# Kernel optimization log

Measured on AMD Instinct MI355X. Metric: run time of the kernel, lower is better.

Reference implementation:

```python
import jax, jax.numpy as jnp
import numpy as np

HIDDEN = 1024
HEADS = 16
HEAD_DIM = HIDDEN // HEADS
ROPE_BASE = 10000.0


def setup_inputs() -> dict:
    key = jax.random.key(0)
    ks = jax.random.split(key, 5)
    B, S = 2, 2048
    x = jax.random.normal(ks[0], (B, S, HIDDEN), dtype=jnp.float32)
    Wqkv_w = jax.random.normal(ks[1], (3 * HIDDEN, HIDDEN), dtype=jnp.float32) * 0.02
    Wqkv_b = jax.random.normal(ks[2], (3 * HIDDEN,), dtype=jnp.float32) * 0.02
    out_w = jax.random.normal(ks[3], (HIDDEN, HIDDEN), dtype=jnp.float32) * 0.02
    out_b = jax.random.normal(ks[4], (HIDDEN,), dtype=jnp.float32) * 0.02
    return {"x": x, "Wqkv_w": Wqkv_w, "Wqkv_b": Wqkv_b, "out_w": out_w, "out_b": out_b}


def _rope_cos_sin(seqlen, dtype):
    inv_freq = 1.0 / (ROPE_BASE ** (jnp.arange(0, HEAD_DIM, 2, dtype=jnp.float32) / HEAD_DIM))
    t = jnp.arange(seqlen, dtype=jnp.float32)
    freqs = jnp.outer(t, inv_freq)                      # [S, D/2]
    emb = jnp.concatenate([freqs, freqs], axis=-1)      # [S, D]
    return jnp.cos(emb).astype(dtype), jnp.sin(emb).astype(dtype)


def _rotate_half(x):
    half = x.shape[-1] // 2
    return jnp.concatenate([-x[..., half:], x[..., :half]], axis=-1)


def reference(x, Wqkv_w, Wqkv_b, out_w, out_b):
    B, S, _ = x.shape
    qkv = x @ Wqkv_w.T + Wqkv_b                          # [B,S,3*H*D]
    qkv = qkv.reshape(B, S, 3, HEADS, HEAD_DIM)
    q, k, v = qkv[:, :, 0], qkv[:, :, 1], qkv[:, :, 2]   # [B,S,H,D]
    cos, sin = _rope_cos_sin(S, x.dtype)
    cos = cos[None, :, None, :]                          # [1,S,1,D]
    sin = sin[None, :, None, :]
    q = q * cos + _rotate_half(q) * sin
    k = k * cos + _rotate_half(k) * sin
    # SDPA (no mask, non-causal): softmax(q k^T / sqrt(D)) v
    scale = 1.0 / jnp.sqrt(jnp.asarray(HEAD_DIM, dtype=x.dtype))
    scores = jnp.einsum('bqhd,bkhd->bhqk', q, k) * scale # [B,H,S,S]
    probs = jax.nn.softmax(scores, axis=-1)
    out = jnp.einsum('bhqk,bkhd->bqhd', probs, v)        # [B,S,H,D]
    out = out.reshape(B, S, HEADS * HEAD_DIM)
    return out @ out_w.T + out_b
```

## Files before the change

kernel.cpp:

```cpp
#include <hip/hip_runtime.h>
#include <hip/hip_bf16.h>
#include <cstdint>

#define HIDDEN 1024
#define HEADS 16
#define HDIM 64
#define BATCH 2
#define SEQ 2048

typedef __attribute__((ext_vector_type(8))) short bfrag;
typedef __attribute__((ext_vector_type(4))) float f32x4;

__device__ inline unsigned short f2bf(float f) {
  unsigned u = __float_as_uint(f);
  return (unsigned short)((u + 0x7FFFu + ((u >> 16) & 1u)) >> 16);
}

__device__ inline void split2(float f, unsigned short& h, unsigned short& l) {
  unsigned u = __float_as_uint(f);
  unsigned hb = (u + 0x7FFFu + ((u >> 16) & 1u)) & 0xFFFF0000u;
  h = (unsigned short)(hb >> 16);
  l = f2bf(f - __uint_as_float(hb));
}

__device__ inline void split8(float4 a, float4 b, float scale, bfrag& hi, bfrag& lo) {
  float v[8] = {a.x, a.y, a.z, a.w, b.x, b.y, b.z, b.w};
  bfrag h, l;
#pragma unroll
  for (int e = 0; e < 8; e++) {
    unsigned short hh, ll;
    split2(v[e] * scale, hh, ll);
    h[e] = (short)hh; l[e] = (short)ll;
  }
  hi = h; lo = l;
}

__global__ __launch_bounds__(256) void rope_table_k(float* __restrict__ ctab,
                                                    float* __restrict__ stab) {
  int idx = blockIdx.x * 256 + threadIdx.x;
  int s = idx >> 5, i = idx & 31;
  float inv = powf(10000.0f, -(float)i / 32.0f);
  float a = (float)s * inv;
  ctab[idx] = cosf(a);
  stab[idx] = sinf(a);
}

__global__ __launch_bounds__(256, 2) void gemm_mfma3(
    const float* __restrict__ A, const float* __restrict__ B,
    const float* __restrict__ bias, float* __restrict__ Cout,
    float* __restrict__ Qb, float* __restrict__ Kb, float* __restrict__ Vb,
    int N, int K, int mode) {
  __shared__ __align__(16) unsigned short Ah[128 * 64];
  __shared__ __align__(16) unsigned short Al[128 * 64];
  __shared__ __align__(16) unsigned short Bh[128 * 64];
  __shared__ __align__(16) unsigned short Bl[128 * 64];

  const int t = threadIdx.x;
  const int lane = t & 63, wv = t >> 6;
  const int wm = wv >> 1, wn = wv & 1;
  const int fr = lane & 15, fg = lane >> 4;
  const int n0 = blockIdx.x * 128, m0 = blockIdx.y * 128;

  f32x4 acc[4][4];
#pragma unroll
  for (int i = 0; i < 4; i++)
#pragma unroll
    for (int j = 0; j < 4; j++) acc[i][j] = (f32x4){0.f, 0.f, 0.f, 0.f};

  float4 fA[4][2], fB[4][2];
#pragma unroll
  for (int it = 0; it < 4; it++) {
    int flat = it * 256 + t, r = flat >> 3, g = flat & 7;
    const float* pa = A + (size_t)(m0 + r) * K + g * 8;
    const float* pb = B + (size_t)(n0 + r) * K + g * 8;
    fA[it][0] = *(const float4*)pa; fA[it][1] = *(const float4*)(pa + 4);
    fB[it][0] = *(const float4*)pb; fB[it][1] = *(const float4*)(pb + 4);
  }

  for (int kt = 0; kt < K; kt += 64) {
    __syncthreads();
#pragma unroll
    for (int it = 0; it < 4; it++) {
      int flat = it * 256 + t, r = flat >> 3, g = flat & 7;
      int ad = r * 64 + ((g ^ (r & 7)) << 3);
      bfrag ha, la, hb, lb;
      split8(fA[it][0], fA[it][1], 1.0f, ha, la);
      split8(fB[it][0], fB[it][1], 1.0f, hb, lb);
      *(bfrag*)&Ah[ad] = ha;
      *(bfrag*)&Al[ad] = la;
      *(bfrag*)&Bh[ad] = hb;
      *(bfrag*)&Bl[ad] = lb;
    }
    __syncthreads();

    if (kt + 64 < K) {
#pragma unroll
      for (int it = 0; it < 4; it++) {
        int flat = it * 256 + t, r = flat >> 3, g = flat & 7;
        const float* pa = A + (size_t)(m0 + r) * K + kt + 64 + g * 8;
        const float* pb = B + (size_t)(n0 + r) * K + kt + 64 + g * 8;
        fA[it][0] = *(const float4*)pa; fA[it][1] = *(const float4*)(pa + 4);
        fB[it][0] = *(const float4*)pb; fB[it][1] = *(const float4*)(pb + 4);
      }
    }

#pragma unroll
    for (int kk = 0; kk < 2; kk++) {
      bfrag ah[4], al[4], bh[4], bl[4];
#pragma unroll
      for (int i = 0; i < 4; i++) {
        int r = wm * 64 + i * 16 + fr;
        int ad = r * 64 + (((kk * 4 + fg) ^ (r & 7)) << 3);
        ah[i] = *(const bfrag*)&Ah[ad];
        al[i] = *(const bfrag*)&Al[ad];
      }
#pragma unroll
      for (int j = 0; j < 4; j++) {
        int r = wn * 64 + j * 16 + fr;
        int ad = r * 64 + (((kk * 4 + fg) ^ (r & 7)) << 3);
        bh[j] = *(const bfrag*)&Bh[ad];
        bl[j] = *(const bfrag*)&Bl[ad];
      }
#pragma unroll
      for (int i = 0; i < 4; i++)
#pragma unroll
        for (int j = 0; j < 4; j++) {
          acc[i][j] = __builtin_amdgcn_mfma_f32_16x16x32_bf16(ah[i], bh[j], acc[i][j], 0, 0, 0);
          acc[i][j] = __builtin_amdgcn_mfma_f32_16x16x32_bf16(ah[i], bl[j], acc[i][j], 0, 0, 0);
          acc[i][j] = __builtin_amdgcn_mfma_f32_16x16x32_bf16(al[i], bh[j], acc[i][j], 0, 0, 0);
        }
    }
  }

#pragma unroll
  for (int j = 0; j < 4; j++) {
    const int n = n0 + wn * 64 + j * 16 + fr;
    const float bb = bias[n];
#pragma unroll
    for (int i = 0; i < 4; i++) {
#pragma unroll
      for (int reg = 0; reg < 4; reg++) {
        const int m = m0 + wm * 64 + i * 16 + fg * 4 + reg;
        const float val = acc[i][j][reg] + bb;
        if (mode == 0) {
          Cout[(size_t)m * N + n] = val;
        } else {
          const int which = n >> 10;
          const int h = (n >> 6) & (HEADS - 1);
          const int d = n & (HDIM - 1);
          const int b = m >> 11, s = m & (SEQ - 1);
          float* base = (which == 0) ? Qb : ((which == 1) ? Kb : Vb);
          base[(((size_t)(b * HEADS + h)) * SEQ + s) * HDIM + d] = val;
        }
      }
    }
  }
}

__global__ __launch_bounds__(256) void rope_apply_k(float* __restrict__ Qb,
                                                    float* __restrict__ Kb,
                                                    const float* __restrict__ ctab,
                                                    const float* __restrict__ stab) {
  int idx = blockIdx.x * 256 + threadIdx.x;
  float* P = blockIdx.y ? Kb : Qb;
  int c4 = (idx & 7) * 4;
  int row = idx >> 3;
  int s = row & (SEQ - 1);
  float* p0 = P + (size_t)row * HDIM + c4;
  float4 lo = *(float4*)p0;
  float4 hi = *(float4*)(p0 + 32);
  float4 cc = *(const float4*)(ctab + s * 32 + c4);
  float4 ss = *(const float4*)(stab + s * 32 + c4);
  float4 nlo, nhi;
  nlo.x = lo.x * cc.x - hi.x * ss.x;  nhi.x = hi.x * cc.x + lo.x * ss.x;
  nlo.y = lo.y * cc.y - hi.y * ss.y;  nhi.y = hi.y * cc.y + lo.y * ss.y;
  nlo.z = lo.z * cc.z - hi.z * ss.z;  nhi.z = hi.z * cc.z + lo.z * ss.z;
  nlo.w = lo.w * cc.w - hi.w * ss.w;  nhi.w = hi.w * cc.w + lo.w * ss.w;
  *(float4*)p0 = nlo;
  *(float4*)(p0 + 32) = nhi;
}

__global__ __launch_bounds__(256, 2) void attn_mfma(
    const float* __restrict__ Qb, const float* __restrict__ Kb,
    const float* __restrict__ Vb, float* __restrict__ Ob) {
  __shared__ __align__(16) unsigned short Kh[64 * 64], Kl[64 * 64];
  __shared__ __align__(16) unsigned short Vth[64 * 64], Vtl[64 * 64];
  __shared__ __align__(16) unsigned short Ph[128 * 64], Pl[128 * 64];

  const int t = threadIdx.x;
  const int lane = t & 63, w = t >> 6;
  const int fr = lane & 15, fg = lane >> 4;
  const int q0 = blockIdx.x * 128;
  const int h = blockIdx.y, b = blockIdx.z;
  const size_t hb = ((size_t)(b * HEADS + h)) * SEQ * HDIM;
  const float* Qp = Qb + hb;
  const float* Kp = Kb + hb;
  const float* Vp = Vb + hb;

  bfrag qh[2][2], ql[2][2];
#pragma unroll
  for (int qf = 0; qf < 2; qf++)
#pragma unroll
    for (int kk = 0; kk < 2; kk++) {
      const float* p = Qp + (size_t)(q0 + w * 32 + qf * 16 + fr) * HDIM + kk * 32 + fg * 8;
      split8(*(const float4*)p, *(const float4*)(p + 4), 0.125f, qh[qf][kk], ql[qf][kk]);
    }

  f32x4 Oacc[2][4];
#pragma unroll
  for (int qf = 0; qf < 2; qf++)
#pragma unroll
    for (int df = 0; df < 4; df++) Oacc[qf][df] = (f32x4){0.f, 0.f, 0.f, 0.f};
  float m_i[2] = {-1e30f, -1e30f}, l_i[2] = {0.f, 0.f};

  for (int kt = 0; kt < SEQ; kt += 64) {
    __syncthreads();
#pragma unroll
    for (int c = 0; c < 2; c++) {
      int flat = c * 256 + t, row = flat >> 3, g = flat & 7;
      const float* p = Kp + (size_t)(kt + row) * HDIM + g * 8;
      bfrag hh, ll;
      split8(*(const float4*)p, *(const float4*)(p + 4), 1.0f, hh, ll);
      int ad = row * 64 + ((g ^ (row & 7)) << 3);
      *(bfrag*)&Kh[ad] = hh;
      *(bfrag*)&Kl[ad] = ll;
    }
#pragma unroll
    for (int c = 0; c < 2; c++) {
      int flat = c * 256 + t, key = flat >> 3, dq = flat & 7;
      const float* p = Vp + (size_t)(kt + key) * HDIM + dq * 8;
      float4 x0 = *(const float4*)p, x1 = *(const float4*)(p + 4);
      float v[8] = {x0.x, x0.y, x0.z, x0.w, x1.x, x1.y, x1.z, x1.w};
#pragma unroll
      for (int e = 0; e < 8; e++) {
        int d = dq * 8 + e;
        unsigned short hh, ll;
        split2(v[e], hh, ll);
        int gs = ((key >> 3) ^ (d & 7) ^ ((d >> 3) & 7)) & 7;
        int ad = d * 64 + gs * 8 + (key & 7);
        Vth[ad] = hh;
        Vtl[ad] = ll;
      }
    }
    __syncthreads();

    f32x4 sacc[4][2];
#pragma unroll
    for (int ki = 0; ki < 4; ki++)
#pragma unroll
      for (int qf = 0; qf < 2; qf++) sacc[ki][qf] = (f32x4){0.f, 0.f, 0.f, 0.f};
#pragma unroll
    for (int kk = 0; kk < 2; kk++) {
      bfrag kh[4], kl[4];
#pragma unroll
      for (int ki = 0; ki < 4; ki++) {
        int row = ki * 16 + fr;
        int ad = row * 64 + (((4 * kk + fg) ^ (row & 7)) << 3);
        kh[ki] = *(const bfrag*)&Kh[ad];
        kl[ki] = *(const bfrag*)&Kl[ad];
      }
#pragma unroll
      for (int ki = 0; ki < 4; ki++)
#pragma unroll
        for (int qf = 0; qf < 2; qf++) {
          sacc[ki][qf] = __builtin_amdgcn_mfma_f32_16x16x32_bf16(kh[ki], qh[qf][kk], sacc[ki][qf], 0, 0, 0);
          sacc[ki][qf] = __builtin_amdgcn_mfma_f32_16x16x32_bf16(kh[ki], ql[qf][kk], sacc[ki][qf], 0, 0, 0);
          sacc[ki][qf] = __builtin_amdgcn_mfma_f32_16x16x32_bf16(kl[ki], qh[qf][kk], sacc[ki][qf], 0, 0, 0);
        }
    }

#pragma unroll
    for (int qf = 0; qf < 2; qf++) {
      float mm = -1e30f;
#pragma unroll
      for (int ki = 0; ki < 4; ki++)
#pragma unroll
        for (int r = 0; r < 4; r++) mm = fmaxf(mm, sacc[ki][qf][r]);
      mm = fmaxf(mm, __shfl_xor(mm, 16));
      mm = fmaxf(mm, __shfl_xor(mm, 32));
      float mn = fmaxf(m_i[qf], mm);
      float alpha = __expf(m_i[qf] - mn);
      m_i[qf] = mn;
      float rs = 0.f;
      float pv[4][4];
#pragma unroll
      for (int ki = 0; ki < 4; ki++)
#pragma unroll
        for (int r = 0; r < 4; r++) {
          float p = __expf(sacc[ki][qf][r] - mn);
          pv[ki][r] = p;
          rs += p;
        }
      rs += __shfl_xor(rs, 16);
      rs += __shfl_xor(rs, 32);
      l_i[qf] = l_i[qf] * alpha + rs;

      int qrow = w * 32 + qf * 16 + fr;
#pragma unroll
      for (int ki = 0; ki < 4; ki++) {
        unsigned short hh[4], ll[4];
#pragma unroll
        for (int r = 0; r < 4; r++) split2(pv[ki][r], hh[r], ll[r]);
        int key0 = ki * 16 + 4 * fg;
        int ads = qrow * 64 + (((key0 >> 3) ^ (qrow & 7)) << 3) + (key0 & 7);
        *(uint2*)&Ph[ads] = make_uint2((unsigned)hh[0] | ((unsigned)hh[1] << 16),
                                       (unsigned)hh[2] | ((unsigned)hh[3] << 16));
        *(uint2*)&Pl[ads] = make_uint2((unsigned)ll[0] | ((unsigned)ll[1] << 16),
                                       (unsigned)ll[2] | ((unsigned)ll[3] << 16));
      }
      float ar[4];
#pragma unroll
      for (int r = 0; r < 4; r++) ar[r] = __shfl(alpha, 4 * fg + r);
#pragma unroll
      for (int df = 0; df < 4; df++)
#pragma unroll
        for (int r = 0; r < 4; r++) Oacc[qf][df][r] *= ar[r];
    }

#pragma unroll
    for (int kk = 0; kk < 2; kk++) {
      bfrag pa[2], pb[2], vh[4], vl[4];
#pragma unroll
      for (int qf = 0; qf < 2; qf++) {
        int qrow = w * 32 + qf * 16 + fr;
        int ad = qrow * 64 + (((4 * kk + fg) ^ (qrow & 7)) << 3);
        pa[qf] = *(const bfrag*)&Ph[ad];
        pb[qf] = *(const bfrag*)&Pl[ad];
      }
#pragma unroll
      for (int df = 0; df < 4; df++) {
        int d = df * 16 + fr;
        int gs = ((4 * kk + fg) ^ (d & 7) ^ ((d >> 3) & 7)) & 7;
        int ad = d * 64 + gs * 8;
        vh[df] = *(const bfrag*)&Vth[ad];
        vl[df] = *(const bfrag*)&Vtl[ad];
      }
#pragma unroll
      for (int qf = 0; qf < 2; qf++)
#pragma unroll
        for (int df = 0; df < 4; df++) {
          Oacc[qf][df] = __builtin_amdgcn_mfma_f32_16x16x32_bf16(pa[qf], vh[df], Oacc[qf][df], 0, 0, 0);
          Oacc[qf][df] = __builtin_amdgcn_mfma_f32_16x16x32_bf16(pa[qf], vl[df], Oacc[qf][df], 0, 0, 0);
          Oacc[qf][df] = __builtin_amdgcn_mfma_f32_16x16x32_bf16(pb[qf], vh[df], Oacc[qf][df], 0, 0, 0);
        }
    }
  }

#pragma unroll
  for (int qf = 0; qf < 2; qf++) {
    float lr[4];
#pragma unroll
    for (int r = 0; r < 4; r++) lr[r] = 1.0f / __shfl(l_i[qf], 4 * fg + r);
#pragma unroll
    for (int df = 0; df < 4; df++)
#pragma unroll
      for (int r = 0; r < 4; r++) {
        int s = q0 + w * 32 + qf * 16 + 4 * fg + r;
        int d = df * 16 + fr;
        Ob[(((size_t)(b * SEQ + s)) * HEADS + h) * HDIM + d] = Oacc[qf][df][r] * lr[r];
      }
  }
}

extern "C" void kernel_launch(void* const* d_in, const int* in_sizes, int n_in,
                              void* d_out, int out_size, void* d_ws, size_t ws_size,
                              hipStream_t stream) {
  const float* x    = (const float*)d_in[0];
  const float* Wqkv = (const float*)d_in[1];
  const float* bqkv = (const float*)d_in[2];
  const float* Wout = (const float*)d_in[3];
  const float* bout = (const float*)d_in[4];
  float* out = (float*)d_out;

  float* ws = (float*)d_ws;
  const size_t HSZ = (size_t)BATCH * HEADS * SEQ * HDIM;
  float* ctab = ws;
  float* stab = ctab + SEQ * 32;
  float* Qb = stab + SEQ * 32;
  float* Kb = Qb + HSZ;
  float* Vb = Kb + HSZ;
  float* Ab = Vb + HSZ;

  hipLaunchKernelGGL(rope_table_k, dim3(SEQ * 32 / 256), dim3(256), 0, stream,
                     ctab, stab);
  hipLaunchKernelGGL(gemm_mfma3, dim3(3 * HIDDEN / 128, BATCH * SEQ / 128),
                     dim3(256), 0, stream,
                     x, Wqkv, bqkv, (float*)nullptr, Qb, Kb, Vb,
                     3 * HIDDEN, HIDDEN, 1);
  hipLaunchKernelGGL(rope_apply_k, dim3(BATCH * HEADS * SEQ * 8 / 256, 2),
                     dim3(256), 0, stream, Qb, Kb, ctab, stab);
  hipLaunchKernelGGL(attn_mfma, dim3(SEQ / 128, HEADS, BATCH), dim3(256), 0, stream,
                     Qb, Kb, Vb, Ab);
  hipLaunchKernelGGL(gemm_mfma3, dim3(HIDDEN / 128, BATCH * SEQ / 128),
                     dim3(256), 0, stream,
                     Ab, Wout, bout, out, (float*)nullptr, (float*)nullptr,
                     (float*)nullptr, HIDDEN, HIDDEN, 0);
}
```

Baseline: 386.6 us.

## Pre-split operands to bf16 hi/lo buffers and stream tiles via global_load_lds

Adds standalone passes that split fp32 inputs, weights, rope-rotated Q/K and a transposed V into swizzled bf16 hi/lo arrays. The GEMM and attention kernels can then load tiles straight into LDS with global_load_lds instead of converting in the main loop. Attention now keeps P in registers, packed with v_cvt_pk_bf16, and feeds it to 16x16x16 MFMAs or lane shuffles instead of staging it in LDS. The GEMM K-tile shrinks to 32 and occupancy rises to 3 blocks per CU. The cost is extra launches and extra global memory traffic for the split buffers, and the weights are re-split on every call.

```diff
diff --git a/kernel.cpp b/kernel.cpp
--- a/kernel.cpp
+++ b/kernel.cpp
@@ -9,30 +9,39 @@
 #define SEQ 2048
 
 typedef __attribute__((ext_vector_type(8))) short bfrag;
+typedef __attribute__((ext_vector_type(4))) short bhalf4;
 typedef __attribute__((ext_vector_type(4))) float f32x4;
+
+union U4B { uint4 u; bfrag b; };
+union U2B { uint2 u; bhalf4 b; };
+
+#if defined(__has_builtin)
+#if __has_builtin(__builtin_amdgcn_mfma_f32_16x16x16bf16_1k)
+#define MFMA16(a, b, c) __builtin_amdgcn_mfma_f32_16x16x16bf16_1k(a, b, c, 0, 0, 0)
+#elif __has_builtin(__builtin_amdgcn_mfma_f32_16x16x16_bf16)
+#define MFMA16(a, b, c) __builtin_amdgcn_mfma_f32_16x16x16_bf16(a, b, c, 0, 0, 0)
+#endif
+#endif
 
 __device__ inline unsigned short f2bf(float f) {
   unsigned u = __float_as_uint(f);
   return (unsigned short)((u + 0x7FFFu + ((u >> 16) & 1u)) >> 16);
 }
-
 __device__ inline void split2(float f, unsigned short& h, unsigned short& l) {
   unsigned u = __float_as_uint(f);
   unsigned hb = (u + 0x7FFFu + ((u >> 16) & 1u)) & 0xFFFF0000u;
   h = (unsigned short)(hb >> 16);
   l = f2bf(f - __uint_as_float(hb));
 }
-
-__device__ inline void split8(float4 a, float4 b, float scale, bfrag& hi, bfrag& lo) {
-  float v[8] = {a.x, a.y, a.z, a.w, b.x, b.y, b.z, b.w};
-  bfrag h, l;
-#pragma unroll
-  for (int e = 0; e < 8; e++) {
-    unsigned short hh, ll;
-    split2(v[e] * scale, hh, ll);
-    h[e] = (short)hh; l[e] = (short)ll;
-  }
-  hi = h; lo = l;
+__device__ inline unsigned cvt_pk_bf16(float a, float b) {
+  unsigned d;
+  asm("v_cvt_pk_bf16_f32 %0, %1, %2" : "=v"(d) : "v"(a), "v"(b));
+  return d;
+}
+__device__ inline void gll16(const void* g, void* l) {
+  __builtin_amdgcn_global_load_lds(
+      (const __attribute__((address_space(1))) void*)g,
+      (__attribute__((address_space(3))) void*)l, 16, 0, 0);
 }
 
 __global__ __launch_bounds__(256) void rope_table_k(float* __restrict__ ctab,
@@ -45,20 +54,39 @@
   stab[idx] = sinf(a);
 }
 
-__global__ __launch_bounds__(256, 2) void gemm_mfma3(
-    const float* __restrict__ A, const float* __restrict__ B,
+__global__ __launch_bounds__(256) void split_swz4(const float* __restrict__ in,
+                                                  ushort* __restrict__ ph,
+                                                  ushort* __restrict__ pl) {
+  int gid = blockIdx.x * 256 + threadIdx.x;
+  int r = gid >> 7, g = gid & 127;
+  const float* p = in + (size_t)r * 1024 + g * 8;
+  float4 a = *(const float4*)p, b = *(const float4*)(p + 4);
+  float v[8] = {a.x, a.y, a.z, a.w, b.x, b.y, b.z, b.w};
+  unsigned hw[4], lw[4];
+#pragma unroll
+  for (int i = 0; i < 4; i++) {
+    unsigned short h0, l0, h1, l1;
+    split2(v[2 * i], h0, l0);
+    split2(v[2 * i + 1], h1, l1);
+    hw[i] = (unsigned)h0 | ((unsigned)h1 << 16);
+    lw[i] = (unsigned)l0 | ((unsigned)l1 << 16);
+  }
+  size_t dst = (size_t)r * 1024 + (g >> 2) * 32 +
+               ((((g & 3) ^ (r & 3) ^ ((r >> 2) & 3))) << 3);
+  *(uint4*)(ph + dst) = make_uint4(hw[0], hw[1], hw[2], hw[3]);
+  *(uint4*)(pl + dst) = make_uint4(lw[0], lw[1], lw[2], lw[3]);
+}
+
+__global__ __launch_bounds__(256, 3) void gemm32(
+    const ushort* __restrict__ aph, const ushort* __restrict__ apl,
+    const ushort* __restrict__ bph, const ushort* __restrict__ bpl,
     const float* __restrict__ bias, float* __restrict__ Cout,
     float* __restrict__ Qb, float* __restrict__ Kb, float* __restrict__ Vb,
-    int N, int K, int mode) {
-  __shared__ __align__(16) unsigned short Ah[128 * 64];
-  __shared__ __align__(16) unsigned short Al[128 * 64];
-  __shared__ __align__(16) unsigned short Bh[128 * 64];
-  __shared__ __align__(16) unsigned short Bl[128 * 64];
-
-  const int t = threadIdx.x;
-  const int lane = t & 63, wv = t >> 6;
-  const int wm = wv >> 1, wn = wv & 1;
-  const int fr = lane & 15, fg = lane >> 4;
+    int N, int mode) {
+  __shared__ __align__(16) ushort Ah[128 * 32], Al[128 * 32];
+  __shared__ __align__(16) ushort Bh[128 * 32], Bl[128 * 32];
+  const int t = threadIdx.x, lane = t & 63, w = t >> 6;
+  const int wm = w >> 1, wn = w & 1, fr = lane & 15, fg = lane >> 4;
   const int n0 = blockIdx.x * 128, m0 = blockIdx.y * 128;
 
   f32x4 acc[4][4];
@@ -67,68 +95,40 @@
 #pragma unroll
     for (int j = 0; j < 4; j++) acc[i][j] = (f32x4){0.f, 0.f, 0.f, 0.f};
 
-  float4 fA[4][2], fB[4][2];
-#pragma unroll
-  for (int it = 0; it < 4; it++) {
-    int flat = it * 256 + t, r = flat >> 3, g = flat & 7;
-    const float* pa = A + (size_t)(m0 + r) * K + g * 8;
-    const float* pb = B + (size_t)(n0 + r) * K + g * 8;
-    fA[it][0] = *(const float4*)pa; fA[it][1] = *(const float4*)(pa + 4);
-    fB[it][0] = *(const float4*)pb; fB[it][1] = *(const float4*)(pb + 4);
-  }
-
-  for (int kt = 0; kt < K; kt += 64) {
+  const ushort* pl4 = (w == 0) ? aph : (w == 1) ? apl : (w == 2) ? bph : bpl;
+  ushort* ld4 = (w == 0) ? Ah : (w == 1) ? Al : (w == 2) ? Bh : Bl;
+  const int rb = (w < 2) ? m0 : n0;
+
+  for (int kt = 0; kt < 1024; kt += 32) {
     __syncthreads();
 #pragma unroll
-    for (int it = 0; it < 4; it++) {
-      int flat = it * 256 + t, r = flat >> 3, g = flat & 7;
-      int ad = r * 64 + ((g ^ (r & 7)) << 3);
-      bfrag ha, la, hb, lb;
-      split8(fA[it][0], fA[it][1], 1.0f, ha, la);
-      split8(fB[it][0], fB[it][1], 1.0f, hb, lb);
-      *(bfrag*)&Ah[ad] = ha;
-      *(bfrag*)&Al[ad] = la;
-      *(bfrag*)&Bh[ad] = hb;
-      *(bfrag*)&Bl[ad] = lb;
+    for (int i = 0; i < 8; i++) {
+      const ushort* src = pl4 + (size_t)(rb + i * 16 + (lane >> 2)) * 1024 +
+                          kt + ((lane & 3) << 3);
+      gll16(src, &ld4[i * 512]);
     }
     __syncthreads();
 
-    if (kt + 64 < K) {
-#pragma unroll
-      for (int it = 0; it < 4; it++) {
-        int flat = it * 256 + t, r = flat >> 3, g = flat & 7;
-        const float* pa = A + (size_t)(m0 + r) * K + kt + 64 + g * 8;
-        const float* pb = B + (size_t)(n0 + r) * K + kt + 64 + g * 8;
-        fA[it][0] = *(const float4*)pa; fA[it][1] = *(const float4*)(pa + 4);
-        fB[it][0] = *(const float4*)pb; fB[it][1] = *(const float4*)(pb + 4);
-      }
-    }
-
-#pragma unroll
-    for (int kk = 0; kk < 2; kk++) {
-      bfrag ah[4], al[4], bh[4], bl[4];
+    bfrag ah[4], al[4];
+#pragma unroll
+    for (int i = 0; i < 4; i++) {
+      int r = wm * 64 + i * 16 + fr;
+      int ad = r * 32 + ((fg ^ (r & 3) ^ ((r >> 2) & 3)) << 3);
+      ah[i] = *(const bfrag*)&Ah[ad];
+      al[i] = *(const bfrag*)&Al[ad];
+    }
+#pragma unroll
+    for (int j = 0; j < 4; j++) {
+      int r = wn * 64 + j * 16 + fr;
+      int ad = r * 32 + ((fg ^ (r & 3) ^ ((r >> 2) & 3)) << 3);
+      bfrag bh = *(const bfrag*)&Bh[ad];
+      bfrag bl = *(const bfrag*)&Bl[ad];
 #pragma unroll
       for (int i = 0; i < 4; i++) {
-        int r = wm * 64 + i * 16 + fr;
-        int ad = r * 64 + (((kk * 4 + fg) ^ (r & 7)) << 3);
-        ah[i] = *(const bfrag*)&Ah[ad];
-        al[i] = *(const bfrag*)&Al[ad];
-      }
-#pragma unroll
-      for (int j = 0; j < 4; j++) {
-        int r = wn * 64 + j * 16 + fr;
-        int ad = r * 64 + (((kk * 4 + fg) ^ (r & 7)) << 3);
-        bh[j] = *(const bfrag*)&Bh[ad];
-        bl[j] = *(const bfrag*)&Bl[ad];
-      }
-#pragma unroll
-      for (int i = 0; i < 4; i++)
-#pragma unroll
-        for (int j = 0; j < 4; j++) {
-          acc[i][j] = __builtin_amdgcn_mfma_f32_16x16x32_bf16(ah[i], bh[j], acc[i][j], 0, 0, 0);
-          acc[i][j] = __builtin_amdgcn_mfma_f32_16x16x32_bf16(ah[i], bl[j], acc[i][j], 0, 0, 0);
-          acc[i][j] = __builtin_amdgcn_mfma_f32_16x16x32_bf16(al[i], bh[j], acc[i][j], 0, 0, 0);
-        }
+        acc[i][j] = __builtin_amdgcn_mfma_f32_16x16x32_bf16(ah[i], bh, acc[i][j], 0, 0, 0);
+        acc[i][j] = __builtin_amdgcn_mfma_f32_16x16x32_bf16(ah[i], bl, acc[i][j], 0, 0, 0);
+        acc[i][j] = __builtin_amdgcn_mfma_f32_16x16x32_bf16(al[i], bh, acc[i][j], 0, 0, 0);
+      }
     }
   }
 
@@ -157,53 +157,121 @@
   }
 }
 
-__global__ __launch_bounds__(256) void rope_apply_k(float* __restrict__ Qb,
-                                                    float* __restrict__ Kb,
-                                                    const float* __restrict__ ctab,
-                                                    const float* __restrict__ stab) {
+__global__ __launch_bounds__(256) void rope_split_k(
+    const float* __restrict__ Qb, const float* __restrict__ Kb,
+    const float* __restrict__ ctab, const float* __restrict__ stab,
+    ushort* __restrict__ Qh, ushort* __restrict__ Ql,
+    ushort* __restrict__ Kh, ushort* __restrict__ Kl) {
   int idx = blockIdx.x * 256 + threadIdx.x;
-  float* P = blockIdx.y ? Kb : Qb;
-  int c4 = (idx & 7) * 4;
-  int row = idx >> 3;
+  int row = idx >> 2, dq = idx & 3;
+  int d0 = dq * 8;
   int s = row & (SEQ - 1);
-  float* p0 = P + (size_t)row * HDIM + c4;
-  float4 lo = *(float4*)p0;
-  float4 hi = *(float4*)(p0 + 32);
-  float4 cc = *(const float4*)(ctab + s * 32 + c4);
-  float4 ss = *(const float4*)(stab + s * 32 + c4);
-  float4 nlo, nhi;
-  nlo.x = lo.x * cc.x - hi.x * ss.x;  nhi.x = hi.x * cc.x + lo.x * ss.x;
-  nlo.y = lo.y * cc.y - hi.y * ss.y;  nhi.y = hi.y * cc.y + lo.y * ss.y;
-  nlo.z = lo.z * cc.z - hi.z * ss.z;  nhi.z = hi.z * cc.z + lo.z * ss.z;
-  nlo.w = lo.w * cc.w - hi.w * ss.w;  nhi.w = hi.w * cc.w + lo.w * ss.w;
-  *(float4*)p0 = nlo;
-  *(float4*)(p0 + 32) = nhi;
-}
-
-__global__ __launch_bounds__(256, 2) void attn_mfma(
-    const float* __restrict__ Qb, const float* __restrict__ Kb,
-    const float* __restrict__ Vb, float* __restrict__ Ob) {
-  __shared__ __align__(16) unsigned short Kh[64 * 64], Kl[64 * 64];
-  __shared__ __align__(16) unsigned short Vth[64 * 64], Vtl[64 * 64];
-  __shared__ __align__(16) unsigned short Ph[128 * 64], Pl[128 * 64];
-
+  const bool isQ = (blockIdx.y == 0);
+  const float* P = (isQ ? Qb : Kb) + (size_t)row * 64;
+  float4 a0 = *(const float4*)(P + d0), a1 = *(const float4*)(P + d0 + 4);
+  float4 b0 = *(const float4*)(P + d0 + 32), b1 = *(const float4*)(P + d0 + 36);
+  float4 c0 = *(const float4*)(ctab + s * 32 + d0), c1 = *(const float4*)(ctab + s * 32 + d0 + 4);
+  float4 s0 = *(const float4*)(stab + s * 32 + d0), s1 = *(const float4*)(stab + s * 32 + d0 + 4);
+  float lo[8] = {a0.x, a0.y, a0.z, a0.w, a1.x, a1.y, a1.z, a1.w};
+  float hi[8] = {b0.x, b0.y, b0.z, b0.w, b1.x, b1.y, b1.z, b1.w};
+  float cc[8] = {c0.x, c0.y, c0.z, c0.w, c1.x, c1.y, c1.z, c1.w};
+  float ss[8] = {s0.x, s0.y, s0.z, s0.w, s1.x, s1.y, s1.z, s1.w};
+  const float sc = isQ ? 0.125f : 1.0f;
+  unsigned lh[4], ll[4], hh[4], hl[4];
+#pragma unroll
+  for (int i = 0; i < 4; i++) {
+    float n0a = (lo[2 * i] * cc[2 * i] - hi[2 * i] * ss[2 * i]) * sc;
+    float n0b = (lo[2 * i + 1] * cc[2 * i + 1] - hi[2 * i + 1] * ss[2 * i + 1]) * sc;
+    float n1a = (hi[2 * i] * cc[2 * i] + lo[2 * i] * ss[2 * i]) * sc;
+    float n1b = (hi[2 * i + 1] * cc[2 * i + 1] + lo[2 * i + 1] * ss[2 * i + 1]) * sc;
+    unsigned short x0, y0, x1, y1;
+    split2(n0a, x0, y0); split2(n0b, x1, y1);
+    lh[i] = (unsigned)x0 | ((unsigned)x1 << 16);
+    ll[i] = (unsigned)y0 | ((unsigned)y1 << 16);
+    split2(n1a, x0, y0); split2(n1b, x1, y1);
+    hh[i] = (unsigned)x0 | ((unsigned)x1 << 16);
+    hl[i] = (unsigned)y0 | ((unsigned)y1 << 16);
+  }
+  size_t base = (size_t)row * 64;
+  if (isQ) {
+    *(uint4*)(Qh + base + d0) = make_uint4(lh[0], lh[1], lh[2], lh[3]);
+    *(uint4*)(Ql + base + d0) = make_uint4(ll[0], ll[1], ll[2], ll[3]);
+    *(uint4*)(Qh + base + d0 + 32) = make_uint4(hh[0], hh[1], hh[2], hh[3]);
+    *(uint4*)(Ql + base + d0 + 32) = make_uint4(hl[0], hl[1], hl[2], hl[3]);
+  } else {
+    int glo = (dq ^ (s & 7)) << 3;
+    int ghi = ((dq + 4) ^ (s & 7)) << 3;
+    *(uint4*)(Kh + base + glo) = make_uint4(lh[0], lh[1], lh[2], lh[3]);
+    *(uint4*)(Kl + base + glo) = make_uint4(ll[0], ll[1], ll[2], ll[3]);
+    *(uint4*)(Kh + base + ghi) = make_uint4(hh[0], hh[1], hh[2], hh[3]);
+    *(uint4*)(Kl + base + ghi) = make_uint4(hl[0], hl[1], hl[2], hl[3]);
+  }
+}
+
+__global__ __launch_bounds__(256) void vtrans_split(const float* __restrict__ Vb,
+                                                    ushort* __restrict__ Vth,
+                                                    ushort* __restrict__ Vtl) {
+  __shared__ float ftile[64][65];
   const int t = threadIdx.x;
-  const int lane = t & 63, w = t >> 6;
+  const int kt = blockIdx.x, bh = blockIdx.y;
+  {
+    int s_loc = t >> 2, dc = (t & 3) * 16;
+    const float* p = Vb + ((size_t)(bh * SEQ) + kt * 64 + s_loc) * 64 + dc;
+#pragma unroll
+    for (int j = 0; j < 4; j++) {
+      float4 v = *(const float4*)(p + j * 4);
+      ftile[s_loc][dc + j * 4 + 0] = v.x;
+      ftile[s_loc][dc + j * 4 + 1] = v.y;
+      ftile[s_loc][dc + j * 4 + 2] = v.z;
+      ftile[s_loc][dc + j * 4 + 3] = v.w;
+    }
+  }
+  __syncthreads();
+  int d = t >> 2, sc = (t & 3) * 16;
+  size_t rowb = ((size_t)(bh * 64 + d)) * SEQ + kt * 64;
+#pragma unroll
+  for (int jg = 0; jg < 2; jg++) {
+    unsigned hw[4], lw[4];
+#pragma unroll
+    for (int i = 0; i < 4; i++) {
+      unsigned short h0, l0, h1, l1;
+      split2(ftile[sc + jg * 8 + 2 * i][d], h0, l0);
+      split2(ftile[sc + jg * 8 + 2 * i + 1][d], h1, l1);
+      hw[i] = (unsigned)h0 | ((unsigned)h1 << 16);
+      lw[i] = (unsigned)l0 | ((unsigned)l1 << 16);
+    }
+    int gsrc = ((sc >> 3) + jg) & 7;
+    int swz = (gsrc ^ (d & 7) ^ ((d >> 3) & 7)) << 3;
+    *(uint4*)(Vth + rowb + swz) = make_uint4(hw[0], hw[1], hw[2], hw[3]);
+    *(uint4*)(Vtl + rowb + swz) = make_uint4(lw[0], lw[1], lw[2], lw[3]);
+  }
+}
+
+__global__ __launch_bounds__(256, 3) void attn_mfma2(
+    const ushort* __restrict__ Qh, const ushort* __restrict__ Ql,
+    const ushort* __restrict__ Kh, const ushort* __restrict__ Kl,
+    const ushort* __restrict__ Vth, const ushort* __restrict__ Vtl,
+    float* __restrict__ Ab) {
+  __shared__ __align__(16) ushort Ks_h[64 * 64], Ks_l[64 * 64];
+  __shared__ __align__(16) ushort Vs_h[64 * 64], Vs_l[64 * 64];
+
+  const int t = threadIdx.x, lane = t & 63, w = t >> 6;
   const int fr = lane & 15, fg = lane >> 4;
   const int q0 = blockIdx.x * 128;
   const int h = blockIdx.y, b = blockIdx.z;
-  const size_t hb = ((size_t)(b * HEADS + h)) * SEQ * HDIM;
-  const float* Qp = Qb + hb;
-  const float* Kp = Kb + hb;
-  const float* Vp = Vb + hb;
+  const int bh = b * HEADS + h;
 
   bfrag qh[2][2], ql[2][2];
 #pragma unroll
   for (int qf = 0; qf < 2; qf++)
 #pragma unroll
     for (int kk = 0; kk < 2; kk++) {
-      const float* p = Qp + (size_t)(q0 + w * 32 + qf * 16 + fr) * HDIM + kk * 32 + fg * 8;
-      split8(*(const float4*)p, *(const float4*)(p + 4), 0.125f, qh[qf][kk], ql[qf][kk]);
+      size_t off = ((size_t)bh * SEQ + q0 + w * 32 + qf * 16 + fr) * 64 + kk * 32 + fg * 8;
+      U4B uh, ul;
+      uh.u = *(const uint4*)(Qh + off);
+      ul.u = *(const uint4*)(Ql + off);
+      qh[qf][kk] = uh.b;
+      ql[qf][kk] = ul.b;
     }
 
   f32x4 Oacc[2][4];
@@ -213,33 +281,26 @@
     for (int df = 0; df < 4; df++) Oacc[qf][df] = (f32x4){0.f, 0.f, 0.f, 0.f};
   float m_i[2] = {-1e30f, -1e30f}, l_i[2] = {0.f, 0.f};
 
+  const int srcA = fr + ((fg & 1) << 5);
+  const int kisel = fg >> 1;
+
   for (int kt = 0; kt < SEQ; kt += 64) {
     __syncthreads();
-#pragma unroll
-    for (int c = 0; c < 2; c++) {
-      int flat = c * 256 + t, row = flat >> 3, g = flat & 7;
-      const float* p = Kp + (size_t)(kt + row) * HDIM + g * 8;
-      bfrag hh, ll;
-      split8(*(const float4*)p, *(const float4*)(p + 4), 1.0f, hh, ll);
-      int ad = row * 64 + ((g ^ (row & 7)) << 3);
-      *(bfrag*)&Kh[ad] = hh;
-      *(bfrag*)&Kl[ad] = ll;
-    }
-#pragma unroll
-    for (int c = 0; c < 2; c++) {
-      int flat = c * 256 + t, key = flat >> 3, dq = flat & 7;
-      const float* p = Vp + (size_t)(kt + key) * HDIM + dq * 8;
-      float4 x0 = *(const float4*)p, x1 = *(const float4*)(p + 4);
-      float v[8] = {x0.x, x0.y, x0.z, x0.w, x1.x, x1.y, x1.z, x1.w};
-#pragma unroll
-      for (int e = 0; e < 8; e++) {
-        int d = dq * 8 + e;
-        unsigned short hh, ll;
-        split2(v[e], hh, ll);
-        int gs = ((key >> 3) ^ (d & 7) ^ ((d >> 3) & 7)) & 7;
-        int ad = d * 64 + gs * 8 + (key & 7);
-        Vth[ad] = hh;
-        Vtl[ad] = ll;
+    if (w < 2) {
+      const ushort* p = w ? Kl : Kh;
+      ushort* ld = w ? Ks_l : Ks_h;
+#pragma unroll
+      for (int i = 0; i < 8; i++) {
+        const ushort* src = p + ((size_t)bh * SEQ + kt + i * 8 + (lane >> 3)) * 64 + ((lane & 7) << 3);
+        gll16(src, &ld[i * 512]);
+      }
+    } else {
+      const ushort* p = (w == 3) ? Vtl : Vth;
+      ushort* ld = (w == 3) ? Vs_l : Vs_h;
+#pragma unroll
+      for (int i = 0; i < 8; i++) {
+        const ushort* src = p + ((size_t)(bh * 64) + i * 8 + (lane >> 3)) * SEQ + kt + ((lane & 7) << 3);
+        gll16(src, &ld[i * 512]);
       }
     }
     __syncthreads();
@@ -251,24 +312,26 @@
       for (int qf = 0; qf < 2; qf++) sacc[ki][qf] = (f32x4){0.f, 0.f, 0.f, 0.f};
 #pragma unroll
     for (int kk = 0; kk < 2; kk++) {
-      bfrag kh[4], kl[4];
 #pragma unroll
       for (int ki = 0; ki < 4; ki++) {
-        int row = ki * 16 + fr;
-        int ad = row * 64 + (((4 * kk + fg) ^ (row & 7)) << 3);
-        kh[ki] = *(const bfrag*)&Kh[ad];
-        kl[ki] = *(const bfrag*)&Kl[ad];
-      }
-#pragma unroll
-      for (int ki = 0; ki < 4; ki++)
+        int r = ki * 16 + fr;
+        int ad = r * 64 + (((kk * 4 + fg) ^ (r & 7)) << 3);
+        bfrag kh = *(const bfrag*)&Ks_h[ad];
+        bfrag kl = *(const bfrag*)&Ks_l[ad];
 #pragma unroll
         for (int qf = 0; qf < 2; qf++) {
-          sacc[ki][qf] = __builtin_amdgcn_mfma_f32_16x16x32_bf16(kh[ki], qh[qf][kk], sacc[ki][qf], 0, 0, 0);
-          sacc[ki][qf] = __builtin_amdgcn_mfma_f32_16x16x32_bf16(kh[ki], ql[qf][kk], sacc[ki][qf], 0, 0, 0);
-          sacc[ki][qf] = __builtin_amdgcn_mfma_f32_16x16x32_bf16(kl[ki], qh[qf][kk], sacc[ki][qf], 0, 0, 0);
-        }
-    }
-
+          sacc[ki][qf] = __builtin_amdgcn_mfma_f32_16x16x32_bf16(kh, qh[qf][kk], sacc[ki][qf], 0, 0, 0);
+          sacc[ki][qf] = __builtin_amdgcn_mfma_f32_16x16x32_bf16(kh, ql[qf][kk], sacc[ki][qf], 0, 0, 0);
+          sacc[ki][qf] = __builtin_amdgcn_mfma_f32_16x16x32_bf16(kl, qh[qf][kk], sacc[ki][qf], 0, 0, 0);
+        }
+      }
+    }
+
+#ifdef MFMA16
+    bhalf4 paH[2][4], paL[2][4];
+#else
+    unsigned phv[2][2][4], plv[2][2][4];
+#endif
 #pragma unroll
     for (int qf = 0; qf < 2; qf++) {
       float mm = -1e30f;
@@ -294,20 +357,34 @@
       rs += __shfl_xor(rs, 16);
       rs += __shfl_xor(rs, 32);
       l_i[qf] = l_i[qf] * alpha + rs;
-
-      int qrow = w * 32 + qf * 16 + fr;
+#ifdef MFMA16
 #pragma unroll
       for (int ki = 0; ki < 4; ki++) {
-        unsigned short hh[4], ll[4];
-#pragma unroll
-        for (int r = 0; r < 4; r++) split2(pv[ki][r], hh[r], ll[r]);
-        int key0 = ki * 16 + 4 * fg;
-        int ads = qrow * 64 + (((key0 >> 3) ^ (qrow & 7)) << 3) + (key0 & 7);
-        *(uint2*)&Ph[ads] = make_uint2((unsigned)hh[0] | ((unsigned)hh[1] << 16),
-                                       (unsigned)hh[2] | ((unsigned)hh[3] << 16));
-        *(uint2*)&Pl[ads] = make_uint2((unsigned)ll[0] | ((unsigned)ll[1] << 16),
-                                       (unsigned)ll[2] | ((unsigned)ll[3] << 16));
-      }
+        unsigned h0 = cvt_pk_bf16(pv[ki][0], pv[ki][1]);
+        unsigned h1 = cvt_pk_bf16(pv[ki][2], pv[ki][3]);
+        float e00 = __uint_as_float(h0 << 16), e01 = __uint_as_float(h0 & 0xFFFF0000u);
+        float e10 = __uint_as_float(h1 << 16), e11 = __uint_as_float(h1 & 0xFFFF0000u);
+        unsigned l0 = cvt_pk_bf16(pv[ki][0] - e00, pv[ki][1] - e01);
+        unsigned l1 = cvt_pk_bf16(pv[ki][2] - e10, pv[ki][3] - e11);
+        U2B th, tl;
+        th.u = make_uint2(h0, h1);
+        tl.u = make_uint2(l0, l1);
+        paH[qf][ki] = th.b;
+        paL[qf][ki] = tl.b;
+      }
+#else
+#pragma unroll
+      for (int ki = 0; ki < 4; ki++)
+#pragma unroll
+        for (int pr = 0; pr < 2; pr++) {
+          float p0 = pv[ki][2 * pr], p1 = pv[ki][2 * pr + 1];
+          unsigned hp = cvt_pk_bf16(p0, p1);
+          float h0 = __uint_as_float(hp << 16);
+          float h1 = __uint_as_float(hp & 0xFFFF0000u);
+          phv[qf][pr][ki] = hp;
+          plv[qf][pr][ki] = cvt_pk_bf16(p0 - h0, p1 - h1);
+        }
+#endif
       float ar[4];
 #pragma unroll
       for (int r = 0; r < 4; r++) ar[r] = __shfl(alpha, 4 * fg + r);
@@ -317,33 +394,60 @@
         for (int r = 0; r < 4; r++) Oacc[qf][df][r] *= ar[r];
     }
 
-#pragma unroll
-    for (int kk = 0; kk < 2; kk++) {
-      bfrag pa[2], pb[2], vh[4], vl[4];
-#pragma unroll
-      for (int qf = 0; qf < 2; qf++) {
-        int qrow = w * 32 + qf * 16 + fr;
-        int ad = qrow * 64 + (((4 * kk + fg) ^ (qrow & 7)) << 3);
-        pa[qf] = *(const bfrag*)&Ph[ad];
-        pb[qf] = *(const bfrag*)&Pl[ad];
-      }
+#ifdef MFMA16
+#pragma unroll
+    for (int ki = 0; ki < 4; ki++) {
+      bhalf4 vh[4], vl[4];
 #pragma unroll
       for (int df = 0; df < 4; df++) {
         int d = df * 16 + fr;
-        int gs = ((4 * kk + fg) ^ (d & 7) ^ ((d >> 3) & 7)) & 7;
-        int ad = d * 64 + gs * 8;
-        vh[df] = *(const bfrag*)&Vth[ad];
-        vl[df] = *(const bfrag*)&Vtl[ad];
+        int ad = d * 64 + ((((2 * ki + (fg >> 1)) ^ (d & 7) ^ ((d >> 3) & 7))) << 3) + ((fg & 1) << 2);
+        vh[df] = *(const bhalf4*)&Vs_h[ad];
+        vl[df] = *(const bhalf4*)&Vs_l[ad];
       }
 #pragma unroll
       for (int qf = 0; qf < 2; qf++)
 #pragma unroll
         for (int df = 0; df < 4; df++) {
-          Oacc[qf][df] = __builtin_amdgcn_mfma_f32_16x16x32_bf16(pa[qf], vh[df], Oacc[qf][df], 0, 0, 0);
-          Oacc[qf][df] = __builtin_amdgcn_mfma_f32_16x16x32_bf16(pa[qf], vl[df], Oacc[qf][df], 0, 0, 0);
-          Oacc[qf][df] = __builtin_amdgcn_mfma_f32_16x16x32_bf16(pb[qf], vh[df], Oacc[qf][df], 0, 0, 0);
-        }
-    }
+          Oacc[qf][df] = MFMA16(paH[qf][ki], vh[df], Oacc[qf][df]);
+          Oacc[qf][df] = MFMA16(paH[qf][ki], vl[df], Oacc[qf][df]);
+          Oacc[qf][df] = MFMA16(paL[qf][ki], vh[df], Oacc[qf][df]);
+        }
+    }
+#else
+#pragma unroll
+    for (int kk = 0; kk < 2; kk++) {
+      bfrag vh[4], vl[4];
+#pragma unroll
+      for (int df = 0; df < 4; df++) {
+        int d = df * 16 + fr;
+        int ad = d * 64 + (((kk * 4 + fg) ^ (d & 7) ^ ((d >> 3) & 7)) << 3);
+        vh[df] = *(const bfrag*)&Vs_h[ad];
+        vl[df] = *(const bfrag*)&Vs_l[ad];
+      }
+#pragma unroll
+      for (int qf = 0; qf < 2; qf++) {
+        U4B pah, pal;
+#pragma unroll
+        for (int wd = 0; wd < 4; wd++) {
+          int src = srcA + ((wd >> 1) << 4);
+          int pr = wd & 1;
+          unsigned a0 = (unsigned)__shfl((int)phv[qf][pr][2 * kk], src);
+          unsigned a1 = (unsigned)__shfl((int)phv[qf][pr][2 * kk + 1], src);
+          unsigned b0 = (unsigned)__shfl((int)plv[qf][pr][2 * kk], src);
+          unsigned b1 = (unsigned)__shfl((int)plv[qf][pr][2 * kk + 1], src);
+          (&pah.u.x)[wd] = kisel ? a1 : a0;
+          (&pal.u.x)[wd] = kisel ? b1 : b0;
+        }
+#pragma unroll
+        for (int df = 0; df < 4; df++) {
+          Oacc[qf][df] = __builtin_amdgcn_mfma_f32_16x16x32_bf16(pah.b, vh[df], Oacc[qf][df], 0, 0, 0);
+          Oacc[qf][df] = __builtin_amdgcn_mfma_f32_16x16x32_bf16(pah.b, vl[df], Oacc[qf][df], 0, 0, 0);
+          Oacc[qf][df] = __builtin_amdgcn_mfma_f32_16x16x32_bf16(pal.b, vh[df], Oacc[qf][df], 0, 0, 0);
+        }
+      }
+    }
+#endif
   }
 
 #pragma unroll
@@ -357,7 +461,7 @@
       for (int r = 0; r < 4; r++) {
         int s = q0 + w * 32 + qf * 16 + 4 * fg + r;
         int d = df * 16 + fr;
-        Ob[(((size_t)(b * SEQ + s)) * HEADS + h) * HDIM + d] = Oacc[qf][df][r] * lr[r];
+        Ab[((size_t)(b * SEQ + s)) * 1024 + h * 64 + d] = Oacc[qf][df][r] * lr[r];
       }
   }
 }
@@ -372,27 +476,42 @@
   const float* bout = (const float*)d_in[4];
   float* out = (float*)d_out;
 
-  float* ws = (float*)d_ws;
-  const size_t HSZ = (size_t)BATCH * HEADS * SEQ * HDIM;
-  float* ctab = ws;
-  float* stab = ctab + SEQ * 32;
-  float* Qb = stab + SEQ * 32;
-  float* Kb = Qb + HSZ;
-  float* Vb = Kb + HSZ;
-  float* Ab = Vb + HSZ;
-
-  hipLaunchKernelGGL(rope_table_k, dim3(SEQ * 32 / 256), dim3(256), 0, stream,
-                     ctab, stab);
-  hipLaunchKernelGGL(gemm_mfma3, dim3(3 * HIDDEN / 128, BATCH * SEQ / 128),
-                     dim3(256), 0, stream,
-                     x, Wqkv, bqkv, (float*)nullptr, Qb, Kb, Vb,
-                     3 * HIDDEN, HIDDEN, 1);
-  hipLaunchKernelGGL(rope_apply_k, dim3(BATCH * HEADS * SEQ * 8 / 256, 2),
-                     dim3(256), 0, stream, Qb, Kb, ctab, stab);
-  hipLaunchKernelGGL(attn_mfma, dim3(SEQ / 128, HEADS, BATCH), dim3(256), 0, stream,
-                     Qb, Kb, Vb, Ab);
-  hipLaunchKernelGGL(gemm_mfma3, dim3(HIDDEN / 128, BATCH * SEQ / 128),
-                     dim3(256), 0, stream,
-                     Ab, Wout, bout, out, (float*)nullptr, (float*)nullptr,
-                     (float*)nullptr, HIDDEN, HIDDEN, 0);
-}
+  char* W = (char*)d_ws;
+  float* ctab = (float*)W;  W += (size_t)SEQ * 32 * 4;
+  float* stab = (float*)W;  W += (size_t)SEQ * 32 * 4;
+  float* Qb   = (float*)W;  W += (size_t)16 << 20;
+  float* Kb   = (float*)W;  W += (size_t)16 << 20;
+  float* Vb   = (float*)W;  W += (size_t)16 << 20;
+  ushort* xh  = (ushort*)W; W += (size_t)8 << 20;
+  ushort* xl  = (ushort*)W; W += (size_t)8 << 20;
+  ushort* wqh = (ushort*)W; W += (size_t)6 << 20;
+  ushort* wql = (ushort*)W; W += (size_t)6 << 20;
+  ushort* woh = (ushort*)W; W += (size_t)2 << 20;
+  ushort* wol = (ushort*)W; W += (size_t)2 << 20;
+  ushort* Khp = (ushort*)W; W += (size_t)8 << 20;
+  ushort* Klp = (ushort*)W; W += (size_t)8 << 20;
+  ushort* Vthp = (ushort*)W; W += (size_t)8 << 20;
+  ushort* Vtlp = (ushort*)W; W += (size_t)8 << 20;
+  ushort* Qhp = xh;
+  ushort* Qlp = xl;
+  float* Abf = Qb;
+  ushort* abh = (ushort*)Kb;
+  ushort* abl = abh + ((size_t)4 << 20);
+
+  hipLaunchKernelGGL(rope_table_k, dim3(SEQ * 32 / 256), dim3(256), 0, stream, ctab, stab);
+  hipLaunchKernelGGL(split_swz4, dim3(4096 / 2), dim3(256), 0, stream, x, xh, xl);
+  hipLaunchKernelGGL(split_swz4, dim3(3072 / 2), dim3(256), 0, stream, Wqkv, wqh, wql);
+  hipLaunchKernelGGL(split_swz4, dim3(1024 / 2), dim3(256), 0, stream, Wout, woh, wol);
+  hipLaunchKernelGGL(gemm32, dim3(3072 / 128, 4096 / 128), dim3(256), 0, stream,
+                     xh, xl, wqh, wql, bqkv, (float*)nullptr, Qb, Kb, Vb, 3072, 1);
+  hipLaunchKernelGGL(rope_split_k, dim3(BATCH * HEADS * SEQ * 4 / 256, 2), dim3(256), 0, stream,
+                     Qb, Kb, ctab, stab, Qhp, Qlp, Khp, Klp);
+  hipLaunchKernelGGL(vtrans_split, dim3(SEQ / 64, BATCH * HEADS), dim3(256), 0, stream,
+                     Vb, Vthp, Vtlp);
+  hipLaunchKernelGGL(attn_mfma2, dim3(SEQ / 128, HEADS, BATCH), dim3(256), 0, stream,
+                     Qhp, Qlp, Khp, Klp, Vthp, Vtlp, Abf);
+  hipLaunchKernelGGL(split_swz4, dim3(4096 / 2), dim3(256), 0, stream, Abf, abh, abl);
+  hipLaunchKernelGGL(gemm32, dim3(1024 / 128, 4096 / 128), dim3(256), 0, stream,
+                     abh, abl, woh, wol, bout, out,
+                     (float*)nullptr, (float*)nullptr, (float*)nullptr, 1024, 0);
+}
```

After: 649.5 us. 68.0% more time.
